# Optimization experiments

Measured on AMD Instinct MI355X. Metric: run time of the kernel, lower is better.

Reference implementation:

```python
import jax, jax.numpy as jnp
import numpy as np

NUM_HEADS = 16
D_MODEL = 1024
D_K = D_MODEL // NUM_HEADS


def setup_inputs() -> dict:
    key = jax.random.key(0)
    ks = jax.random.split(key, 11)
    B, S = 2, 2048
    s = 1.0 / np.sqrt(D_MODEL)
    return {
        "Q": jax.random.normal(ks[0], (B, S, D_MODEL), jnp.float32),
        "K": jax.random.normal(ks[1], (B, S, D_MODEL), jnp.float32),
        "V": jax.random.normal(ks[2], (B, S, D_MODEL), jnp.float32),
        "Wq": jax.random.normal(ks[3], (D_MODEL, D_MODEL), jnp.float32) * s,
        "bq": jnp.zeros((D_MODEL,), jnp.float32),
        "Wk": jax.random.normal(ks[4], (D_MODEL, D_MODEL), jnp.float32) * s,
        "bk": jnp.zeros((D_MODEL,), jnp.float32),
        "Wv": jax.random.normal(ks[5], (D_MODEL, D_MODEL), jnp.float32) * s,
        "bv": jnp.zeros((D_MODEL,), jnp.float32),
        "Wo": jax.random.normal(ks[6], (D_MODEL, D_MODEL), jnp.float32) * s,
        "bo": jnp.zeros((D_MODEL,), jnp.float32),
    }


def _split_heads(x):
    B, S, _ = x.shape
    return x.reshape(B, S, NUM_HEADS, D_K).transpose(0, 2, 1, 3)  # (B,H,S,Dk)


def reference(Q, K, V, Wq, bq, Wk, bk, Wv, bv, Wo, bo):
    q = _split_heads(Q @ Wq + bq)
    k = _split_heads(K @ Wk + bk)
    v = _split_heads(V @ Wv + bv)
    scores = jnp.einsum("bhqd,bhkd->bhqk", q, k) / jnp.sqrt(jnp.asarray(D_K, q.dtype))
    attn = jax.nn.softmax(scores, axis=-1)
    out = jnp.einsum("bhqk,bhkd->bhqd", attn, v)  # (B,H,S,Dk)
    B, H, S, Dk = out.shape
    combined = out.transpose(0, 2, 1, 3).reshape(B, S, H * Dk)
    return combined @ Wo + bo
```

## Files before the change

### kernel.cpp

```cpp
#include <hip/hip_runtime.h>
#include <stdint.h>

#define DM   1024
#define NH   16
#define DKH  64
#define SEQ  2048
#define NB   2

typedef __attribute__((ext_vector_type(8))) short  frag8;
typedef __attribute__((ext_vector_type(4))) short  frag4;
typedef __attribute__((ext_vector_type(4))) short  short4v;
typedef __attribute__((ext_vector_type(8))) short  short8v;
typedef __attribute__((ext_vector_type(4))) float  f32x4;

__device__ __forceinline__ unsigned short f2bf(float x){
  unsigned u = __float_as_uint(x);
  u += 0x7fffu + ((u >> 16) & 1u);
  return (unsigned short)(u >> 16);
}

__device__ __forceinline__ float dev_exp2(float x){
  return __builtin_amdgcn_exp2f(x);
}

#define GLOAD16(GP, LP) __builtin_amdgcn_global_load_lds( \
    (__attribute__((address_space(1))) void*)(GP), \
    (__attribute__((address_space(3))) void*)(LP), 16, 0, 0)


__global__ __launch_bounds__(256) void cast_qkv(const float* __restrict__ Q,
                                                const float* __restrict__ K,
                                                const float* __restrict__ V,
                                                short* __restrict__ dst){
  const int z = blockIdx.z;
  const float* src = (z == 0) ? Q : (z == 1 ? K : V);
  const int i = (blockIdx.x * 256 + threadIdx.x) * 4;
  float4 f = *(const float4*)(src + i);
  short4v s;
  s.x = (short)f2bf(f.x); s.y = (short)f2bf(f.y);
  s.z = (short)f2bf(f.z); s.w = (short)f2bf(f.w);
  *(short4v*)(dst + (long)z * (SEQ*NB*DM) + i) = s;
}

__global__ __launch_bounds__(256) void wtrans(const float* __restrict__ Wq,
                                              const float* __restrict__ Wk,
                                              const float* __restrict__ Wv,
                                              const float* __restrict__ Wo,
                                              short* __restrict__ wt){
  const int z = blockIdx.z;
  const float* W = (z == 0) ? Wq : (z == 1 ? Wk : (z == 2 ? Wv : Wo));
  short* out = wt + (long)z * (DM*DM);
  __shared__ float t[32][33];
  const int n0 = blockIdx.x * 32, k0 = blockIdx.y * 32;
  const int c = threadIdx.x & 31, r0 = threadIdx.x >> 5;
#pragma unroll
  for (int i = 0; i < 4; ++i){
    int r = r0 + i * 8;
    t[r][c] = W[(k0 + r) * DM + n0 + c];
  }
  __syncthreads();
#pragma unroll
  for (int i = 0; i < 4; ++i){
    int r = r0 + i * 8;
    out[(n0 + r) * DM + k0 + c] = (short)f2bf(t[c][r]);
  }
}

__device__ __forceinline__ void store_out(short* p, float v){ *p = (short)f2bf(v); }
__device__ __forceinline__ void store_out(float* p, float v){ *p = v; }

template<typename OT>
__global__ __launch_bounds__(256) void gemm_bt(const short* __restrict__ Abase, long Astride,
                                               const short* __restrict__ Btbase, long Btstride,
                                               const float* __restrict__ bias0,
                                               const float* __restrict__ bias1,
                                               const float* __restrict__ bias2,
                                               OT* __restrict__ Cbase, long Cstride,
                                               float qscale){
  const int z = blockIdx.z;
  const short* A  = Abase + (long)z * Astride;
  const short* Bt = Btbase + (long)z * Btstride;
  OT* C = Cbase + (long)z * Cstride;
  const float* bias = (z == 0) ? bias0 : (z == 1 ? bias1 : bias2);
  const float scale = (z == 0) ? qscale : 1.0f;
  const int KD = DM, ND = DM;

  __shared__ __align__(16) short As[128 * 64];
  __shared__ __align__(16) short Bs[128 * 64];

  const int tid = threadIdx.x;
  const int w = tid >> 6, lane = tid & 63, l15 = lane & 15, quad = lane >> 4;
  const int wy = w >> 1, wx = w & 1;
  const int bm = blockIdx.x * 128, bn = blockIdx.y * 128;
  const int lrow = lane >> 3;
  const int lcolsw = (((lane & 7) ^ lrow) & 7) * 8;

  f32x4 acc[4][4] = {};

  for (int kt = 0; kt < KD; kt += 64){
#pragma unroll
    for (int i = 0; i < 4; ++i){
      int j = w * 4 + i;
      GLOAD16(A  + (bm + j * 8 + lrow) * KD + kt + lcolsw, &As[j * 512]);
      GLOAD16(Bt + (bn + j * 8 + lrow) * KD + kt + lcolsw, &Bs[j * 512]);
    }
    __syncthreads();
#pragma unroll
    for (int ks = 0; ks < 2; ++ks){
      frag8 af[4], bf_[4];
#pragma unroll
      for (int mt = 0; mt < 4; ++mt)
        af[mt] = *(const frag8*)&As[(wy * 64 + mt * 16 + l15) * 64 +
                                    (((ks * 4 + quad) ^ (l15 & 7)) * 8)];
#pragma unroll
      for (int nt = 0; nt < 4; ++nt)
        bf_[nt] = *(const frag8*)&Bs[(wx * 64 + nt * 16 + l15) * 64 +
                                     (((ks * 4 + quad) ^ (l15 & 7)) * 8)];
#pragma unroll
      for (int mt = 0; mt < 4; ++mt)
#pragma unroll
        for (int nt = 0; nt < 4; ++nt)
          acc[mt][nt] = __builtin_amdgcn_mfma_f32_16x16x32_bf16(af[mt], bf_[nt], acc[mt][nt], 0, 0, 0);
    }
    __syncthreads();
  }

#pragma unroll
  for (int mt = 0; mt < 4; ++mt){
#pragma unroll
    for (int r = 0; r < 4; ++r){
      int m = bm + wy * 64 + mt * 16 + quad * 4 + r;
#pragma unroll
      for (int nt = 0; nt < 4; ++nt){
        int n = bn + wx * 64 + nt * 16 + l15;
        float v = (acc[mt][nt][r] + bias[n]) * scale;
        store_out(&C[(long)m * ND + n], v);
      }
    }
  }
}

template<typename OT>
__global__ __launch_bounds__(256) void gemm64_bt(const short* __restrict__ A,
                                                 const short* __restrict__ Bt,
                                                 const float* __restrict__ bias,
                                                 OT* __restrict__ C,
                                                 float scale){
  const int KD = DM, ND = DM;
  __shared__ __align__(16) short As[64 * 64];
  __shared__ __align__(16) short Bs[128 * 64];
  const int tid = threadIdx.x;
  const int w = tid >> 6, lane = tid & 63, l15 = lane & 15, quad = lane >> 4;
  const int wy = w >> 1, wx = w & 1;
  const int bm = blockIdx.x * 64, bn = blockIdx.y * 128;
  const int lrow = lane >> 3;
  const int lcolsw = (((lane & 7) ^ lrow) & 7) * 8;
  f32x4 acc[2][4] = {};

  for (int kt = 0; kt < KD; kt += 64){
#pragma unroll
    for (int i = 0; i < 2; ++i){
      int j = w * 2 + i;
      GLOAD16(A + (bm + j * 8 + lrow) * KD + kt + lcolsw, &As[j * 512]);
    }
#pragma unroll
    for (int i = 0; i < 4; ++i){
      int j = w * 4 + i;
      GLOAD16(Bt + (bn + j * 8 + lrow) * KD + kt + lcolsw, &Bs[j * 512]);
    }
    __syncthreads();
#pragma unroll
    for (int ks = 0; ks < 2; ++ks){
      frag8 af[2], bf_[4];
#pragma unroll
      for (int mt = 0; mt < 2; ++mt)
        af[mt] = *(const frag8*)&As[(wy * 32 + mt * 16 + l15) * 64 +
                                    (((ks * 4 + quad) ^ (l15 & 7)) * 8)];
#pragma unroll
      for (int nt = 0; nt < 4; ++nt)
        bf_[nt] = *(const frag8*)&Bs[(wx * 64 + nt * 16 + l15) * 64 +
                                     (((ks * 4 + quad) ^ (l15 & 7)) * 8)];
#pragma unroll
      for (int mt = 0; mt < 2; ++mt)
#pragma unroll
        for (int nt = 0; nt < 4; ++nt)
          acc[mt][nt] = __builtin_amdgcn_mfma_f32_16x16x32_bf16(af[mt], bf_[nt], acc[mt][nt], 0, 0, 0);
    }
    __syncthreads();
  }

#pragma unroll
  for (int mt = 0; mt < 2; ++mt){
#pragma unroll
    for (int r = 0; r < 4; ++r){
      int m = bm + wy * 32 + mt * 16 + quad * 4 + r;
#pragma unroll
      for (int nt = 0; nt < 4; ++nt){
        int n = bn + wx * 64 + nt * 16 + l15;
        store_out(&C[(long)m * ND + n], (acc[mt][nt][r] + bias[n]) * scale);
      }
    }
  }
}

__global__ __launch_bounds__(256) void vtrans(const short* __restrict__ v,
                                              short* __restrict__ vt){
  const int bh = blockIdx.y;
  const int b = bh >> 4, h = bh & 15;
  const int s0 = blockIdx.x * 64;
  __shared__ short tT[64][66];
  const short* vb = v + ((long)(b * SEQ + s0)) * DM + h * DKH;
  for (int j = threadIdx.x; j < 512; j += 256){
    int row = j >> 3, off = (j & 7) * 8;
    short8v d = *(const short8v*)(vb + row * DM + off);
#pragma unroll
    for (int e = 0; e < 8; ++e) tT[off + e][row] = d[e];
  }
  __syncthreads();
  short* out = vt + (long)bh * (DKH * SEQ) + s0;
  for (int j = threadIdx.x; j < 512; j += 256){
    int dr = j >> 3, soff = (j & 7) * 8;
    short8v o;
#pragma unroll
    for (int e = 0; e < 8; ++e) o[e] = tT[dr][soff + e];
    *(short8v*)(out + dr * SEQ + soff) = o;
  }
}

__global__ __launch_bounds__(256) void flash(const short* __restrict__ q,
                                             const short* __restrict__ k,
                                             const short* __restrict__ vt,
                                             short* __restrict__ comb){
  const int bh = blockIdx.y;
  const int b = bh >> 4, h = bh & 15;
  const int q0 = blockIdx.x * 128;
  const int tid = threadIdx.x;
  const int w = tid >> 6, lane = tid & 63, l15 = lane & 15, quad = lane >> 4;

  __shared__ __align__(16) short Ks[64 * 64];
  __shared__ __align__(16) short Vs[64 * 64];

  frag8 aq[2][2];
  const short* qb = q + ((long)(b * SEQ + q0 + w * 32)) * DM + h * DKH;
#pragma unroll
  for (int mt = 0; mt < 2; ++mt)
#pragma unroll
    for (int ks = 0; ks < 2; ++ks)
      aq[mt][ks] = *(const frag8*)(qb + (mt * 16 + l15) * DM + ks * 32 + quad * 8);

  frag4 ones4;
#pragma unroll
  for (int e = 0; e < 4; ++e) ones4[e] = (short)0x3F80;

  f32x4 O[2][4] = {};
  f32x4 Lacc[2] = {{0.f,0.f,0.f,0.f},{0.f,0.f,0.f,0.f}};

  const short* kb  = k + ((long)b * SEQ) * DM + h * DKH;
  const short* vtb = vt + (long)bh * (DKH * SEQ);
  const int lrow8 = lane >> 3;
  const int lcolsw = (((lane & 7) ^ lrow8) & 7) * 8;

  for (int kt = 0; kt < SEQ / 64; ++kt){
#pragma unroll
    for (int i = 0; i < 2; ++i){
      int jj = w * 2 + i;
      GLOAD16(kb + (kt * 64 + jj * 8 + lrow8) * DM + lcolsw, &Ks[jj * 512]);
      GLOAD16(vtb + (jj * 8 + lrow8) * SEQ + kt * 64 + lcolsw, &Vs[jj * 512]);
    }
    __syncthreads();

    f32x4 scT[2][4];
#pragma unroll
    for (int mt = 0; mt < 2; ++mt)
#pragma unroll
      for (int nt = 0; nt < 4; ++nt) scT[mt][nt] = (f32x4){0.f, 0.f, 0.f, 0.f};
#pragma unroll
    for (int ks = 0; ks < 2; ++ks){
#pragma unroll
      for (int nt = 0; nt < 4; ++nt){
        frag8 ak = *(const frag8*)&Ks[(nt * 16 + l15) * 64 +
                                      (((ks * 4 + quad) ^ (l15 & 7)) * 8)];
#pragma unroll
        for (int mt = 0; mt < 2; ++mt)
          scT[mt][nt] = __builtin_amdgcn_mfma_f32_16x16x32_bf16(ak, aq[mt][ks], scT[mt][nt], 0, 0, 0);
      }
    }

    frag4 ap[2][4];
#pragma unroll
    for (int mt = 0; mt < 2; ++mt)
#pragma unroll
      for (int nt = 0; nt < 4; ++nt){
#pragma unroll
        for (int r = 0; r < 4; ++r){
          float e = dev_exp2(scT[mt][nt][r]);
          ap[mt][nt][r] = (short)((__float_as_uint(e) + 0x8000u) >> 16);
        }
      }

#pragma unroll
    for (int nt = 0; nt < 4; ++nt){
#pragma unroll
      for (int dt = 0; dt < 4; ++dt){
        frag4 bv4 = *(const frag4*)&Vs[(dt * 16 + l15) * 64 +
                                       (((nt * 2 + (quad >> 1)) ^ (l15 & 7)) * 8) +
                                       (quad & 1) * 4];
#pragma unroll
        for (int mt = 0; mt < 2; ++mt)
          O[mt][dt] = __builtin_amdgcn_mfma_f32_16x16x16bf16_1k(ap[mt][nt], bv4, O[mt][dt], 0, 0, 0);
      }
#pragma unroll
      for (int mt = 0; mt < 2; ++mt)
        Lacc[mt] = __builtin_amdgcn_mfma_f32_16x16x16bf16_1k(ap[mt][nt], ones4, Lacc[mt], 0, 0, 0);
    }
    __syncthreads();
  }

  short* ob = comb + ((long)(b * SEQ + q0 + w * 32)) * DM + h * DKH;
#pragma unroll
  for (int mt = 0; mt < 2; ++mt){
#pragma unroll
    for (int r = 0; r < 4; ++r){
      float inv = 1.f / Lacc[mt][r];
#pragma unroll
      for (int nt = 0; nt < 4; ++nt)
        ob[(mt * 16 + quad * 4 + r) * DM + nt * 16 + l15] = (short)f2bf(O[mt][nt][r] * inv);
    }
  }
}

extern "C" void kernel_launch(void* const* d_in, const int* in_sizes, int n_in,
                              void* d_out, int out_size, void* d_ws, size_t ws_size,
                              hipStream_t stream){
  const float* Q  = (const float*)d_in[0];
  const float* K  = (const float*)d_in[1];
  const float* V  = (const float*)d_in[2];
  const float* Wq = (const float*)d_in[3];
  const float* bq = (const float*)d_in[4];
  const float* Wk = (const float*)d_in[5];
  const float* bk = (const float*)d_in[6];
  const float* Wv = (const float*)d_in[7];
  const float* bv = (const float*)d_in[8];
  const float* Wo = (const float*)d_in[9];
  const float* bo = (const float*)d_in[10];
  float* out = (float*)d_out;

  const long TEN = (long)NB * SEQ * DM;
  const long WEL = (long)DM * DM;
  short* ws   = (short*)d_ws;
  short* xc   = ws;
  short* wt   = xc + 3 * TEN;
  short* qkv  = wt + 4 * WEL;
  short* vtr  = qkv + 3 * TEN;
  short* comb = vtr + TEN;

  cast_qkv<<<dim3(4096, 1, 3), 256, 0, stream>>>(Q, K, V, xc);
  wtrans<<<dim3(32, 32, 4), 256, 0, stream>>>(Wq, Wk, Wv, Wo, wt);
  gemm_bt<short><<<dim3(32, 8, 3), 256, 0, stream>>>(xc, TEN, wt, WEL, bq, bk, bv,
                                                     qkv, TEN, 0.125f * 1.44269504f);
  vtrans<<<dim3(32, 32), 256, 0, stream>>>(qkv + 2 * TEN, vtr);
  flash<<<dim3(16, 32), 256, 0, stream>>>(qkv, qkv + TEN, vtr, comb);
  gemm64_bt<float><<<dim3(64, 8), 256, 0, stream>>>(comb, wt + 3 * WEL, bo, out, 1.0f);
  (void)in_sizes; (void)n_in; (void)out_size; (void)ws_size;
}
```

Before: 243.4 us.

## Triple-buffer K/V tiles in flash attention with async prefetch two tiles ahead

Moves the flash kernel's K and V staging from a single LDS buffer loaded and waited on every iteration to a three-deep ring. Asynchronous global_load_lds prefetches run two tiles ahead, and explicit vmcnt waits plus raw s_barrier calls replace the full __syncthreads. It also raises wave priority with s_setprio around the MFMA compute section. The aim is to hide global load latency behind the matrix work. In exchange LDS per block grows threefold, which can lower occupancy, and correctness now depends on hand-counted vmcnt values.

Result: faster. 235.5 us (-3.2%).

```diff
diff --git a/kernel.cpp b/kernel.cpp
--- a/kernel.cpp
+++ b/kernel.cpp
@@ -26,6 +26,9 @@
 #define GLOAD16(GP, LP) __builtin_amdgcn_global_load_lds( \
     (__attribute__((address_space(1))) void*)(GP), \
     (__attribute__((address_space(3))) void*)(LP), 16, 0, 0)
+
+#define LDSFENCE() do{ asm volatile("" ::: "memory"); \
+                       __builtin_amdgcn_sched_barrier(0); }while(0)
 
 
 __global__ __launch_bounds__(256) void cast_qkv(const float* __restrict__ Q,
@@ -237,8 +240,8 @@
   const int tid = threadIdx.x;
   const int w = tid >> 6, lane = tid & 63, l15 = lane & 15, quad = lane >> 4;
 
-  __shared__ __align__(16) short Ks[64 * 64];
-  __shared__ __align__(16) short Vs[64 * 64];
+  __shared__ __align__(16) short Ks[3][64 * 64];
+  __shared__ __align__(16) short Vs[3][64 * 64];
 
   frag8 aq[2][2];
   const short* qb = q + ((long)(b * SEQ + q0 + w * 32)) * DM + h * DKH;
@@ -260,61 +263,85 @@
   const int lrow8 = lane >> 3;
   const int lcolsw = (((lane & 7) ^ lrow8) & 7) * 8;
 
-  for (int kt = 0; kt < SEQ / 64; ++kt){
-#pragma unroll
-    for (int i = 0; i < 2; ++i){
-      int jj = w * 2 + i;
-      GLOAD16(kb + (kt * 64 + jj * 8 + lrow8) * DM + lcolsw, &Ks[jj * 512]);
-      GLOAD16(vtb + (jj * 8 + lrow8) * SEQ + kt * 64 + lcolsw, &Vs[jj * 512]);
-    }
-    __syncthreads();
-
-    f32x4 scT[2][4];
-#pragma unroll
-    for (int mt = 0; mt < 2; ++mt)
-#pragma unroll
-      for (int nt = 0; nt < 4; ++nt) scT[mt][nt] = (f32x4){0.f, 0.f, 0.f, 0.f};
-#pragma unroll
-    for (int ks = 0; ks < 2; ++ks){
-#pragma unroll
-      for (int nt = 0; nt < 4; ++nt){
-        frag8 ak = *(const frag8*)&Ks[(nt * 16 + l15) * 64 +
-                                      (((ks * 4 + quad) ^ (l15 & 7)) * 8)];
-#pragma unroll
-        for (int mt = 0; mt < 2; ++mt)
-          scT[mt][nt] = __builtin_amdgcn_mfma_f32_16x16x32_bf16(ak, aq[mt][ks], scT[mt][nt], 0, 0, 0);
-      }
-    }
-
-    frag4 ap[2][4];
-#pragma unroll
-    for (int mt = 0; mt < 2; ++mt)
-#pragma unroll
-      for (int nt = 0; nt < 4; ++nt){
-#pragma unroll
-        for (int r = 0; r < 4; ++r){
-          float e = dev_exp2(scT[mt][nt][r]);
-          ap[mt][nt][r] = (short)((__float_as_uint(e) + 0x8000u) >> 16);
-        }
-      }
-
-#pragma unroll
-    for (int nt = 0; nt < 4; ++nt){
-#pragma unroll
-      for (int dt = 0; dt < 4; ++dt){
-        frag4 bv4 = *(const frag4*)&Vs[(dt * 16 + l15) * 64 +
-                                       (((nt * 2 + (quad >> 1)) ^ (l15 & 7)) * 8) +
-                                       (quad & 1) * 4];
-#pragma unroll
-        for (int mt = 0; mt < 2; ++mt)
-          O[mt][dt] = __builtin_amdgcn_mfma_f32_16x16x16bf16_1k(ap[mt][nt], bv4, O[mt][dt], 0, 0, 0);
-      }
-#pragma unroll
-      for (int mt = 0; mt < 2; ++mt)
-        Lacc[mt] = __builtin_amdgcn_mfma_f32_16x16x16bf16_1k(ap[mt][nt], ones4, Lacc[mt], 0, 0, 0);
-    }
-    __syncthreads();
-  }
+#define STAGE(KT, BSEL) do{                                                     \
+  _Pragma("unroll")                                                             \
+  for (int i_ = 0; i_ < 2; ++i_){                                               \
+    int jj_ = w * 2 + i_;                                                       \
+    GLOAD16(kb + ((KT) * 64 + jj_ * 8 + lrow8) * DM + lcolsw,                   \
+            &Ks[BSEL][jj_ * 512]);                                              \
+    GLOAD16(vtb + (jj_ * 8 + lrow8) * SEQ + (KT) * 64 + lcolsw,                 \
+            &Vs[BSEL][jj_ * 512]);                                              \
+  } }while(0)
+
+#define COMPUTE(BS) do{                                                         \
+  __builtin_amdgcn_s_setprio(1);                                                \
+  f32x4 scT[2][4];                                                              \
+  _Pragma("unroll") for (int mt = 0; mt < 2; ++mt)                              \
+    _Pragma("unroll") for (int nt = 0; nt < 4; ++nt)                            \
+      scT[mt][nt] = (f32x4){0.f, 0.f, 0.f, 0.f};                                \
+  _Pragma("unroll") for (int ks = 0; ks < 2; ++ks){                             \
+    _Pragma("unroll") for (int nt = 0; nt < 4; ++nt){                           \
+      frag8 ak = *(const frag8*)&Ks[BS][(nt * 16 + l15) * 64 +                  \
+                                        (((ks * 4 + quad) ^ (l15 & 7)) * 8)];   \
+      _Pragma("unroll") for (int mt = 0; mt < 2; ++mt)                          \
+        scT[mt][nt] = __builtin_amdgcn_mfma_f32_16x16x32_bf16(                  \
+            ak, aq[mt][ks], scT[mt][nt], 0, 0, 0);                              \
+    }                                                                           \
+  }                                                                             \
+  frag4 ap[2][4];                                                               \
+  _Pragma("unroll") for (int mt = 0; mt < 2; ++mt)                              \
+    _Pragma("unroll") for (int nt = 0; nt < 4; ++nt){                           \
+      _Pragma("unroll") for (int r = 0; r < 4; ++r){                            \
+        float e = dev_exp2(scT[mt][nt][r]);                                     \
+        ap[mt][nt][r] = (short)((__float_as_uint(e) + 0x8000u) >> 16);          \
+      }                                                                         \
+    }                                                                           \
+  _Pragma("unroll") for (int nt = 0; nt < 4; ++nt){                             \
+    _Pragma("unroll") for (int dt = 0; dt < 4; ++dt){                           \
+      frag4 bv4 = *(const frag4*)&Vs[BS][(dt * 16 + l15) * 64 +                 \
+                                   (((nt * 2 + (quad >> 1)) ^ (l15 & 7)) * 8) + \
+                                   (quad & 1) * 4];                             \
+      _Pragma("unroll") for (int mt = 0; mt < 2; ++mt)                          \
+        O[mt][dt] = __builtin_amdgcn_mfma_f32_16x16x16bf16_1k(                  \
+            ap[mt][nt], bv4, O[mt][dt], 0, 0, 0);                               \
+    }                                                                           \
+    _Pragma("unroll") for (int mt = 0; mt < 2; ++mt)                            \
+      Lacc[mt] = __builtin_amdgcn_mfma_f32_16x16x16bf16_1k(                     \
+          ap[mt][nt], ones4, Lacc[mt], 0, 0, 0);                                \
+  }                                                                             \
+  __builtin_amdgcn_s_setprio(0);                                                \
+}while(0)
+
+#define ITER(KT, BC, BSNEXT) do{                                                \
+  STAGE((KT) + 2, BSNEXT);                                                      \
+  asm volatile("s_waitcnt vmcnt(8)" ::: "memory");                              \
+  __builtin_amdgcn_s_barrier();                                                 \
+  LDSFENCE();                                                                   \
+  COMPUTE(BC);                                                                  \
+  asm volatile("s_waitcnt lgkmcnt(0)" ::: "memory");                            \
+  __builtin_amdgcn_sched_barrier(0);                                            \
+  __builtin_amdgcn_s_barrier();                                                 \
+}while(0)
+
+  STAGE(0, 0);
+  STAGE(1, 1);
+  for (int kt = 0; kt < SEQ / 64 - 2; kt += 3){
+    ITER(kt,     0, 2);
+    ITER(kt + 1, 1, 0);
+    ITER(kt + 2, 2, 1);
+  }
+  asm volatile("s_waitcnt vmcnt(4)" ::: "memory");
+  __builtin_amdgcn_s_barrier();
+  LDSFENCE();
+  COMPUTE(0);
+  asm volatile("s_waitcnt vmcnt(0)" ::: "memory");
+  __builtin_amdgcn_s_barrier();
+  LDSFENCE();
+  COMPUTE(1);
+
+#undef ITER
+#undef COMPUTE
+#undef STAGE
 
   short* ob = comb + ((long)(b * SEQ + q0 + w * 32)) * DM + h * DKH;
 #pragma unroll
```
